# Kernel tuning notes

Measured on AMD Instinct MI355X. Metric: run time of the kernel, lower is better.

Reference implementation:

```python
import jax, jax.numpy as jnp
import numpy as np


def setup_inputs() -> dict:
    key = jax.random.key(0)
    k1, k2 = jax.random.split(key)
    x = jax.random.normal(k1, (8, 64, 224, 224), dtype=jnp.float32)
    kernel = jax.random.normal(k2, (64, 1, 3, 3), dtype=jnp.float32)
    return {"x": x, "kernel": kernel, "stride": 1, "padding": 1, "dilation": 1}


def reference(x, kernel, stride, padding, dilation):
    # Tropical-max (morphological dilation) conv: out[b,c,i,j] =
    #   max_{ki,kj} x_pad[b,c,i*stride+ki*dilation, j*stride+kj*dilation] + kernel[c,0,ki,kj]
    # Padding uses the tropical neutral element -inf, matching the torch module.
    B, C, H, W = x.shape
    O, _, K, _ = kernel.shape
    out_h = (H + 2 * padding - dilation * (K - 1) - 1) // stride + 1
    out_w = (W + 2 * padding - dilation * (K - 1) - 1) // stride + 1
    neutral = -jnp.inf
    xp = jnp.pad(x, ((0, 0), (0, 0), (padding, padding), (padding, padding)),
                 constant_values=neutral)
    # Initialize at -inf: equivalent to the module's extra neutral pad on the K axis.
    acc = jnp.full((B, C, out_h, out_w), neutral, dtype=x.dtype)
    h_span = (out_h - 1) * stride + 1
    w_span = (out_w - 1) * stride + 1
    # Small fixed K*K loop over kernel taps; avoids materializing the unfolded tensor.
    for ki in range(K):
        for kj in range(K):
            patch = jax.lax.slice(
                xp,
                (0, 0, ki * dilation, kj * dilation),
                (B, C, ki * dilation + h_span, kj * dilation + w_span),
                (1, 1, stride, stride),
            )  # [B, C, out_h, out_w]
            acc = jnp.maximum(acc, patch + kernel[None, :, 0, ki, kj, None, None])
    return acc
```

## Files before the change

kernel.cpp:

```cpp
#include <hip/hip_runtime.h>
#include <math.h>


#define H_DIM 224
#define W_DIM 224
#define W4 56
#define C_DIM 64

__global__ __launch_bounds__(256) void tropical_conv_kernel(
    const float* __restrict__ x,
    const float* __restrict__ kern,
    float* __restrict__ out,
    int total)
{
    int idx = blockIdx.x * blockDim.x + threadIdx.x;
    if (idx >= total) return;

    const float NEG = -INFINITY;

    int j4 = idx % W4;
    int t  = idx / W4;
    int i  = t % H_DIM;
    int bc = t / H_DIM;
    int c  = bc & (C_DIM - 1);

    const float* kc    = kern + c * 9;
    const float* plane = x + (size_t)bc * (H_DIM * W_DIM);
    int j0 = j4 * 4;

    float4 acc = make_float4(NEG, NEG, NEG, NEG);

    #pragma unroll
    for (int ki = 0; ki < 3; ++ki) {
        int r = i + ki - 1;
        if (r < 0 || r >= H_DIM) continue;
        const float* row = plane + r * W_DIM;

        float4 a    = *(const float4*)(row + j0);
        float left  = (j4 > 0)        ? row[j0 - 1] : NEG;
        float right = (j4 < W4 - 1)   ? row[j0 + 4] : NEG;

        float k0 = kc[ki * 3 + 0];
        float k1 = kc[ki * 3 + 1];
        float k2 = kc[ki * 3 + 2];

        acc.x = fmaxf(acc.x, fmaxf(fmaxf(left + k0, a.x + k1), a.y  + k2));
        acc.y = fmaxf(acc.y, fmaxf(fmaxf(a.x  + k0, a.y + k1), a.z  + k2));
        acc.z = fmaxf(acc.z, fmaxf(fmaxf(a.y  + k0, a.z + k1), a.w  + k2));
        acc.w = fmaxf(acc.w, fmaxf(fmaxf(a.z  + k0, a.w + k1), right + k2));
    }

    float4* op = (float4*)(out + (size_t)bc * (H_DIM * W_DIM) + (size_t)i * W_DIM + j0);
    *op = acc;
}

extern "C" void kernel_launch(void* const* d_in, const int* in_sizes, int n_in,
                              void* d_out, int out_size, void* d_ws, size_t ws_size,
                              hipStream_t stream) {
    const float* x    = (const float*)d_in[0];
    const float* kern = (const float*)d_in[1];
    float* out        = (float*)d_out;

    const int total = 8 * C_DIM * H_DIM * W4;
    const int block = 256;
    const int grid  = (total + block - 1) / block;
    tropical_conv_kernel<<<grid, block, 0, stream>>>(x, kern, out, total);
}
```

Measured before the change: 206.3 us.

## Stage 18-row input strips in LDS via async global-to-LDS copies

Result: faster. 188.8 us (-8.5%).

```diff
diff --git a/kernel.cpp b/kernel.cpp
--- a/kernel.cpp
+++ b/kernel.cpp
@@ -5,53 +5,106 @@
 #define H_DIM 224
 #define W_DIM 224
 #define W4 56
+#define STRIP 16
+#define TILES_PER_PLANE 14
 #define C_DIM 64
+#define NEG (-INFINITY)
+
+#define LDS_ROWS 18
+#define LDS_DW (LDS_ROWS * W_DIM)
+#define LDS_PAD 8
+
+typedef float f4 __attribute__((ext_vector_type(4)));
+
+typedef __attribute__((address_space(3))) void       lds_void;
+typedef __attribute__((address_space(1))) const void gbl_void;
+
+__device__ __forceinline__ void async_copy16(const float* g, float* l) {
+    __builtin_amdgcn_global_load_lds((gbl_void*)g, (lds_void*)l, 16, 0, 0);
+}
+
+__device__ __forceinline__ float m3(float a, float b, float c) {
+    return fmaxf(fmaxf(a, b), c);
+}
 
 __global__ __launch_bounds__(256) void tropical_conv_kernel(
     const float* __restrict__ x,
     const float* __restrict__ kern,
-    float* __restrict__ out,
-    int total)
+    float* __restrict__ out)
 {
-    int idx = blockIdx.x * blockDim.x + threadIdx.x;
-    if (idx >= total) return;
+    __shared__ float lds[LDS_DW + LDS_PAD];
 
-    const float NEG = -INFINITY;
+    int b   = blockIdx.x;
+    int g   = b % TILES_PER_PLANE;
+    int bc  = b / TILES_PER_PLANE;
+    int c   = bc & (C_DIM - 1);
+    int tid = threadIdx.x;
 
-    int j4 = idx % W4;
-    int t  = idx / W4;
-    int i  = t % H_DIM;
-    int bc = t / H_DIM;
-    int c  = bc & (C_DIM - 1);
+    const float* plane  = x   + (size_t)bc * (H_DIM * W_DIM);
+    float*       oplane = out + (size_t)bc * (H_DIM * W_DIM);
 
-    const float* kc    = kern + c * 9;
-    const float* plane = x + (size_t)bc * (H_DIM * W_DIM);
-    int j0 = j4 * 4;
+    int r0         = g * STRIP - 1;
+    int nrows      = LDS_ROWS;
+    int lds_off_dw = 0;
+    if (g == 0)                       { r0 = 0; nrows = 17; lds_off_dw = W_DIM; }
+    else if (g == TILES_PER_PLANE - 1) { nrows = 17; }
 
-    float4 acc = make_float4(NEG, NEG, NEG, NEG);
+    const float* gsrc = plane + (size_t)r0 * W_DIM;
+    int nchunk = nrows * (W_DIM / 4);
+    for (int k = tid; k < nchunk; k += 256) {
+        async_copy16(gsrc + k * 4, &lds[lds_off_dw + k * 4]);
+    }
+    if (g == 0) {
+        if (tid < W_DIM) lds[tid] = NEG;
+    } else if (g == TILES_PER_PLANE - 1) {
+        if (tid < W_DIM) lds[(LDS_ROWS - 1) * W_DIM + tid] = NEG;
+    }
+    __syncthreads();
+
+    const float* kc = kern + c * 9;
+    float k00 = kc[0], k01 = kc[1], k02 = kc[2];
+    float k10 = kc[3], k11 = kc[4], k12 = kc[5];
+    float k20 = kc[6], k21 = kc[7], k22 = kc[8];
 
     #pragma unroll
-    for (int ki = 0; ki < 3; ++ki) {
-        int r = i + ki - 1;
-        if (r < 0 || r >= H_DIM) continue;
-        const float* row = plane + r * W_DIM;
+    for (int it = 0; it < 4; ++it) {
+        int o = it * 256 + tid;
+        if (o < STRIP * W4) {
+            int r  = o / W4;
+            int cc = o % W4;
+            int base = r * W_DIM + cc * 4;
+            bool hl = (cc > 0), hr = (cc < W4 - 1);
+            int li = base - (hl ? 1 : 0);
 
-        float4 a    = *(const float4*)(row + j0);
-        float left  = (j4 > 0)        ? row[j0 - 1] : NEG;
-        float right = (j4 < W4 - 1)   ? row[j0 + 4] : NEG;
+            f4 a0 = *(const f4*)&lds[base];
+            f4 a1 = *(const f4*)&lds[base + W_DIM];
+            f4 a2 = *(const f4*)&lds[base + 2 * W_DIM];
+            float l0 = lds[li];
+            float l1 = lds[li + W_DIM];
+            float l2 = lds[li + 2 * W_DIM];
+            float q0 = lds[base + 4];
+            float q1 = lds[base + W_DIM + 4];
+            float q2 = lds[base + 2 * W_DIM + 4];
+            if (!hl) { l0 = NEG; l1 = NEG; l2 = NEG; }
+            if (!hr) { q0 = NEG; q1 = NEG; q2 = NEG; }
 
-        float k0 = kc[ki * 3 + 0];
-        float k1 = kc[ki * 3 + 1];
-        float k2 = kc[ki * 3 + 2];
+            f4 acc;
+            acc.x = m3(m3(l0   + k00, a0.x + k01, a0.y + k02),
+                       m3(l1   + k10, a1.x + k11, a1.y + k12),
+                       m3(l2   + k20, a2.x + k21, a2.y + k22));
+            acc.y = m3(m3(a0.x + k00, a0.y + k01, a0.z + k02),
+                       m3(a1.x + k10, a1.y + k11, a1.z + k12),
+                       m3(a2.x + k20, a2.y + k21, a2.z + k22));
+            acc.z = m3(m3(a0.y + k00, a0.z + k01, a0.w + k02),
+                       m3(a1.y + k10, a1.z + k11, a1.w + k12),
+                       m3(a2.y + k20, a2.z + k21, a2.w + k22));
+            acc.w = m3(m3(a0.z + k00, a0.w + k01, q0   + k02),
+                       m3(a1.z + k10, a1.w + k11, q1   + k12),
+                       m3(a2.z + k20, a2.w + k21, q2   + k22));
 
-        acc.x = fmaxf(acc.x, fmaxf(fmaxf(left + k0, a.x + k1), a.y  + k2));
-        acc.y = fmaxf(acc.y, fmaxf(fmaxf(a.x  + k0, a.y + k1), a.z  + k2));
-        acc.z = fmaxf(acc.z, fmaxf(fmaxf(a.y  + k0, a.z + k1), a.w  + k2));
-        acc.w = fmaxf(acc.w, fmaxf(fmaxf(a.z  + k0, a.w + k1), right + k2));
+            *(f4*)(oplane + (size_t)(g * STRIP + r) * W_DIM + cc * 4) = acc;
+        }
     }
-
-    float4* op = (float4*)(out + (size_t)bc * (H_DIM * W_DIM) + (size_t)i * W_DIM + j0);
-    *op = acc;
 }
 
 extern "C" void kernel_launch(void* const* d_in, const int* in_sizes, int n_in,
@@ -61,8 +114,6 @@
     const float* kern = (const float*)d_in[1];
     float* out        = (float*)d_out;
 
-    const int total = 8 * C_DIM * H_DIM * W4;
-    const int block = 256;
-    const int grid  = (total + block - 1) / block;
-    tropical_conv_kernel<<<grid, block, 0, stream>>>(x, kern, out, total);
+    const int grid = 8 * C_DIM * TILES_PER_PLANE;
+    tropical_conv_kernel<<<grid, 256, 0, stream>>>(x, kern, out);
 }
```

## Stage row strips in LDS with async double-buffered loads and register row reuse

Applied to the files above, without the earlier changes.

Result: faster. 192.3 us (-6.8%).

```diff
diff --git a/kernel.cpp b/kernel.cpp
--- a/kernel.cpp
+++ b/kernel.cpp
@@ -5,53 +5,121 @@
 #define H_DIM 224
 #define W_DIM 224
 #define W4 56
+#define STRIP 16
+#define TILES_PER_PLANE 14
 #define C_DIM 64
+#define NTILES (8 * C_DIM * TILES_PER_PLANE)
+#define TPB 7
+#define NBLK (NTILES / TPB)
+#define NEG (-INFINITY)
+
+#define LROWS 18
+#define LDW (LROWS * W_DIM)
+#define LSTRIDE (LDW + 8)
+
+typedef float f4 __attribute__((ext_vector_type(4)));
+typedef __attribute__((address_space(3))) void       lds_void;
+typedef __attribute__((address_space(1))) const void gbl_void;
+
+__device__ __forceinline__ void async16(const float* g, float* l) {
+    __builtin_amdgcn_global_load_lds((gbl_void*)g, (lds_void*)l, 16, 0, 0);
+}
+__device__ __forceinline__ float m3(float a, float b, float c) {
+    return fmaxf(fmaxf(a, b), c);
+}
 
 __global__ __launch_bounds__(256) void tropical_conv_kernel(
     const float* __restrict__ x,
-    const float* __restrict__ kern,
-    float* __restrict__ out,
-    int total)
+    const float* __restrict__ kw,
+    float* __restrict__ out)
 {
-    int idx = blockIdx.x * blockDim.x + threadIdx.x;
-    if (idx >= total) return;
+    __shared__ __align__(16) float lds_raw[2][LSTRIDE];
 
-    const float NEG = -INFINITY;
+    int tid   = threadIdx.x;
+    int tile0 = blockIdx.x * TPB;
 
-    int j4 = idx % W4;
-    int t  = idx / W4;
-    int i  = t % H_DIM;
-    int bc = t / H_DIM;
-    int c  = bc & (C_DIM - 1);
+    auto issue_copy = [&](int tile, int parity) {
+        float* buf = &lds_raw[parity][4];
+        int g  = tile % TILES_PER_PLANE;
+        int bc = tile / TILES_PER_PLANE;
+        const float* plane = x + (size_t)bc * (H_DIM * W_DIM);
+        int r0 = g * STRIP - 1, nrows = LROWS, off = 0;
+        if (g == 0)                        { r0 = 0; nrows = 17; off = W_DIM; }
+        else if (g == TILES_PER_PLANE - 1) { nrows = 17; }
+        const float* gsrc = plane + (size_t)r0 * W_DIM;
+        int nchunk = nrows * (W_DIM / 4);
+        for (int k = tid; k < nchunk; k += 256)
+            async16(gsrc + k * 4, buf + off + k * 4);
+        if (g == 0)                        { if (tid < W_DIM) buf[tid] = NEG; }
+        else if (g == TILES_PER_PLANE - 1) { if (tid < W_DIM) buf[(LROWS - 1) * W_DIM + tid] = NEG; }
+    };
 
-    const float* kc    = kern + c * 9;
-    const float* plane = x + (size_t)bc * (H_DIM * W_DIM);
-    int j0 = j4 * 4;
+    issue_copy(tile0, 0);
+    __syncthreads();
 
-    float4 acc = make_float4(NEG, NEG, NEG, NEG);
+    int s  = tid / W4;
+    int cc = tid % W4;
+    bool active = (tid < 224);
+    bool hl = (cc > 0), hr = (cc < W4 - 1);
 
-    #pragma unroll
-    for (int ki = 0; ki < 3; ++ki) {
-        int r = i + ki - 1;
-        if (r < 0 || r >= H_DIM) continue;
-        const float* row = plane + r * W_DIM;
+    for (int it = 0; it < TPB; ++it) {
+        int tile = tile0 + it;
+        float* cur = &lds_raw[it & 1][4];
+        if (it + 1 < TPB) issue_copy(tile + 1, (it + 1) & 1);
 
-        float4 a    = *(const float4*)(row + j0);
-        float left  = (j4 > 0)        ? row[j0 - 1] : NEG;
-        float right = (j4 < W4 - 1)   ? row[j0 + 4] : NEG;
+        int g  = tile % TILES_PER_PLANE;
+        int bc = tile / TILES_PER_PLANE;
+        int c  = bc & (C_DIM - 1);
+        const float* kc = kw + c * 9;
+        float k00 = kc[0], k01 = kc[1], k02 = kc[2];
+        float k10 = kc[3], k11 = kc[4], k12 = kc[5];
+        float k20 = kc[6], k21 = kc[7], k22 = kc[8];
+        float* orow0 = out + (size_t)bc * (H_DIM * W_DIM)
+                           + (size_t)(g * STRIP + s * 4) * W_DIM + cc * 4;
 
-        float k0 = kc[ki * 3 + 0];
-        float k1 = kc[ki * 3 + 1];
-        float k2 = kc[ki * 3 + 2];
+        if (active) {
+            f4 hk0_2, hk0_1, hk1_1;
+            #pragma unroll
+            for (int j = 0; j < 6; ++j) {
+                int a = (s * 4 + j) * W_DIM + cc * 4;
+                f4 A = *(const f4*)&cur[a - 4];
+                f4 B = *(const f4*)&cur[a];
+                f4 C = *(const f4*)&cur[a + 4];
+                float w0 = hl ? A.w : NEG;
+                float w1 = B.x, w2 = B.y, w3 = B.z, w4 = B.w;
+                float w5 = hr ? C.x : NEG;
 
-        acc.x = fmaxf(acc.x, fmaxf(fmaxf(left + k0, a.x + k1), a.y  + k2));
-        acc.y = fmaxf(acc.y, fmaxf(fmaxf(a.x  + k0, a.y + k1), a.z  + k2));
-        acc.z = fmaxf(acc.z, fmaxf(fmaxf(a.y  + k0, a.z + k1), a.w  + k2));
-        acc.w = fmaxf(acc.w, fmaxf(fmaxf(a.z  + k0, a.w + k1), right + k2));
+                f4 hk0, hk1, hk2;
+                if (j <= 3) {
+                    hk0.x = m3(w0 + k00, w1 + k01, w2 + k02);
+                    hk0.y = m3(w1 + k00, w2 + k01, w3 + k02);
+                    hk0.z = m3(w2 + k00, w3 + k01, w4 + k02);
+                    hk0.w = m3(w3 + k00, w4 + k01, w5 + k02);
+                }
+                if (j >= 1 && j <= 4) {
+                    hk1.x = m3(w0 + k10, w1 + k11, w2 + k12);
+                    hk1.y = m3(w1 + k10, w2 + k11, w3 + k12);
+                    hk1.z = m3(w2 + k10, w3 + k11, w4 + k12);
+                    hk1.w = m3(w3 + k10, w4 + k11, w5 + k12);
+                }
+                if (j >= 2) {
+                    hk2.x = m3(w0 + k20, w1 + k21, w2 + k22);
+                    hk2.y = m3(w1 + k20, w2 + k21, w3 + k22);
+                    hk2.z = m3(w2 + k20, w3 + k21, w4 + k22);
+                    hk2.w = m3(w3 + k20, w4 + k21, w5 + k22);
+
+                    f4 o;
+                    o.x = m3(hk0_2.x, hk1_1.x, hk2.x);
+                    o.y = m3(hk0_2.y, hk1_1.y, hk2.y);
+                    o.z = m3(hk0_2.z, hk1_1.z, hk2.z);
+                    o.w = m3(hk0_2.w, hk1_1.w, hk2.w);
+                    *(f4*)(orow0 + (size_t)(j - 2) * W_DIM) = o;
+                }
+                hk0_2 = hk0_1; hk0_1 = hk0; hk1_1 = hk1;
+            }
+        }
+        __syncthreads();
     }
-
-    float4* op = (float4*)(out + (size_t)bc * (H_DIM * W_DIM) + (size_t)i * W_DIM + j0);
-    *op = acc;
 }
 
 extern "C" void kernel_launch(void* const* d_in, const int* in_sizes, int n_in,
@@ -61,8 +129,5 @@
     const float* kern = (const float*)d_in[1];
     float* out        = (float*)d_out;
 
-    const int total = 8 * C_DIM * H_DIM * W4;
-    const int block = 256;
-    const int grid  = (total + block - 1) / block;
-    tropical_conv_kernel<<<grid, block, 0, stream>>>(x, kern, out, total);
+    tropical_conv_kernel<<<NBLK, 256, 0, stream>>>(x, kern, out);
 }
```
